# Kernel tuning notes

Measured on AMD Instinct MI355X. Metric: run time of the kernel, lower is better.

The kernel has to match this reference:

```python
import jax, jax.numpy as jnp
import numpy as np

B, L, N_PATCH, NUM_Q, C_IN, C_OUT = 32, 40, 2304, 100, 768, 256


def setup_inputs() -> dict:
    key = jax.random.key(0)
    ks = jax.random.split(key, 7)
    text_feat = jax.random.normal(ks[0], (B, L, C_IN), jnp.float32)
    img_feat = jax.random.normal(ks[1], (B, N_PATCH, C_IN), jnp.float32)
    # text_scores in (0,1): scale fns use log(1.22 - x), valid for x < 1.22
    text_scores = jax.random.uniform(ks[2], (B, 1), jnp.float32, 0.01, 0.99)
    text_mask = jax.random.randint(ks[3], (B, L), 0, 2).astype(jnp.int32)
    # guarantee at least a few unmasked text tokens per row (avoid all -inf)
    text_mask = text_mask.at[:, :4].set(0)
    dummy_token = jax.random.normal(ks[4], (1, NUM_Q, C_IN), jnp.float32)
    Wq = jax.random.normal(ks[5], (C_OUT, C_IN), jnp.float32) / np.sqrt(C_IN).astype(np.float32)
    bq = jnp.zeros((C_OUT,), jnp.float32)
    return dict(text_feat=text_feat, img_feat=img_feat, text_scores=text_scores,
                text_mask=text_mask, dummy_token=dummy_token, Wq=Wq, bq=bq)


def _l2norm(x, eps=1e-8):
    n = jnp.linalg.norm(x, axis=-1, keepdims=True)
    return x / jnp.maximum(n, eps)


def reference(text_feat, img_feat, text_scores, text_mask, dummy_token, Wq, bq):
    b, n_patch, c = img_feat.shape
    num_q = dummy_token.shape[1]
    l = text_feat.shape[1]

    # img features with learned dummy tokens appended: [B, N+Q, C]
    img_all = jnp.concatenate(
        [img_feat, jnp.broadcast_to(dummy_token, (b, num_q, c))], axis=1)

    # cosine similarity between every (patch|dummy) and every text token: [B, N+Q, L]
    cos = jnp.einsum('bpc,blc->bpl', _l2norm(img_all), _l2norm(text_feat))
    sim_norm = (cos + 1.0) * 0.5

    # custom log-based scale factors from text confidence score ([B,1])
    log_term = jnp.log(1.22 - text_scores)            # [B, 1]
    not_dummy = -0.59 * log_term + 0.12               # applied to real patches
    dummy = 0.59 * log_term + 0.88                    # applied to dummy tokens
    scale_factor = jnp.concatenate(
        [jnp.broadcast_to(not_dummy[:, :, None], (b, n_patch, l)),
         jnp.broadcast_to(dummy[:, :, None], (b, num_q, l))], axis=1)

    scaled = scale_factor * sim_norm                  # [B, N+Q, L]
    scaled = jnp.where(text_mask[:, None, :].astype(bool), -jnp.inf, scaled)

    # masked max over text tokens, then topk over patches (+dummies)
    max_per_patch = jnp.max(scaled, axis=-1)          # [B, N+Q]
    _, topk_idx = jax.lax.top_k(max_per_patch, num_q)  # [B, Q]

    # gather selected features (equivalent to one-hot scatter + bmm in torch)
    selected = jnp.take_along_axis(img_all, topk_idx[:, :, None], axis=1)  # [B,Q,C]
    query = selected @ Wq.T + bq                      # [B, Q, C_OUT]
    return query, topk_idx, sim_norm, scaled
```

## Files before the change

### kernel.cpp

```cpp
#include <hip/hip_runtime.h>
#include <math.h>

#define B_    32
#define L_    40
#define PIMG  2304
#define NQ    100
#define PALL  2404
#define C_    768
#define COUT  256
#define NT    24
#define TP    64

#define NEG_INF (-__builtin_huge_valf())
#define MASK_SENTINEL (-3.0e38f)

typedef short s16x8 __attribute__((ext_vector_type(8)));
typedef float f32x4 __attribute__((ext_vector_type(4)));

#define BSTR 40

__device__ __forceinline__ unsigned cvtpk(float a, float b) {
    unsigned r;
    asm("v_cvt_pk_bf16_f32 %0, %1, %2" : "=v"(r) : "v"(a), "v"(b));
    return r;
}
__device__ __forceinline__ void cvt44u(float4 v, uint2* h, uint2* l) {
    unsigned h01 = cvtpk(v.x, v.y);
    unsigned h23 = cvtpk(v.z, v.w);
    *h = make_uint2(h01, h23);
    *l = make_uint2(
        cvtpk(v.x - __uint_as_float(h01 << 16), v.y - __uint_as_float(h01 & 0xFFFF0000u)),
        cvtpk(v.z - __uint_as_float(h23 << 16), v.w - __uint_as_float(h23 & 0xFFFF0000u)));
}
union U4S8 { uint4 u; s16x8 s; };
__device__ __forceinline__ void split8(float4 v0, float4 v1, s16x8& h, s16x8& l) {
    unsigned h0 = cvtpk(v0.x, v0.y);
    unsigned h1 = cvtpk(v0.z, v0.w);
    unsigned h2 = cvtpk(v1.x, v1.y);
    unsigned h3 = cvtpk(v1.z, v1.w);
    unsigned l0 = cvtpk(v0.x - __uint_as_float(h0 << 16), v0.y - __uint_as_float(h0 & 0xFFFF0000u));
    unsigned l1 = cvtpk(v0.z - __uint_as_float(h1 << 16), v0.w - __uint_as_float(h1 & 0xFFFF0000u));
    unsigned l2 = cvtpk(v1.x - __uint_as_float(h2 << 16), v1.y - __uint_as_float(h2 & 0xFFFF0000u));
    unsigned l3 = cvtpk(v1.z - __uint_as_float(h3 << 16), v1.w - __uint_as_float(h3 & 0xFFFF0000u));
    U4S8 uh; uh.u = make_uint4(h0, h1, h2, h3); h = uh.s;
    U4S8 ul; ul.u = make_uint4(l0, l1, l2, l3); l = ul.s;
}
__device__ __forceinline__ float dot4(float4 v) {
    return v.x * v.x + v.y * v.y + v.z * v.z + v.w * v.w;
}

__device__ __forceinline__ void gl16(const float* g, float* lds_base) {
#if __has_builtin(__builtin_amdgcn_global_load_lds)
    __builtin_amdgcn_global_load_lds(
        (const __attribute__((address_space(1))) void*)g,
        (__attribute__((address_space(3))) void*)lds_base, 16, 0, 0);
#else
    const int lane = threadIdx.x & 63;
    *(float4*)((char*)lds_base + lane * 16) = *(const float4*)g;
#endif
}

#define MFMA3(ACC, AH, AL, BH, BL) do { \
    ACC = __builtin_amdgcn_mfma_f32_16x16x32_bf16(AH, BH, ACC, 0, 0, 0); \
    ACC = __builtin_amdgcn_mfma_f32_16x16x32_bf16(AH, BL, ACC, 0, 0, 0); \
    ACC = __builtin_amdgcn_mfma_f32_16x16x32_bf16(AL, BH, ACC, 0, 0, 0); \
} while (0)

__global__ void k_textnorm(const float* __restrict__ text, float* __restrict__ invT,
                           const float* __restrict__ scores,
                           float* __restrict__ sA, float* __restrict__ sB) {
    int t    = threadIdx.x;
    if (blockIdx.x == 0 && t < B_) {
        float s  = scores[t];
        float lt = logf(1.22f - s);
        sA[t] = -0.59f * lt + 0.12f;
        sB[t] =  0.59f * lt + 0.88f;
    }
    int row  = blockIdx.x * 4 + (t >> 6);
    int lane = t & 63;
    const float* src = text + (size_t)row * C_;
    float ss = 0.f;
#pragma unroll
    for (int j = 0; j < 12; ++j) {
        float x = src[lane + 64 * j];
        ss += x * x;
    }
#pragma unroll
    for (int m = 1; m < 64; m <<= 1) ss += __shfl_xor(ss, m);
    if (lane == 0) invT[row] = 1.0f / fmaxf(sqrtf(ss), 1e-8f);
}

__global__ __launch_bounds__(256) void k_main(
    const float* __restrict__ img,  const float* __restrict__ dummy,
    const float* __restrict__ text, const float* __restrict__ invT,
    const int*  __restrict__ mask,  const float* __restrict__ scaleA,
    const float* __restrict__ scaleB, float* __restrict__ simn,
    float* __restrict__ scld, float* __restrict__ maxpp)
{
    __shared__ float  Af[2][TP * 32];
    __shared__ ushort Bh[2][L_][BSTR], Bl[2][L_][BSTR];
    __shared__ float  invT_s[48];
    __shared__ int    mask_s[48];

    const int t    = threadIdx.x;
    const int b    = blockIdx.y;
    const int p0   = blockIdx.x * TP;
    const int lane = t & 63, w = t >> 6;
    const int lr   = lane & 15, kg = lane >> 4;

    if (t < 48) {
        invT_s[t] = (t < L_) ? invT[b * L_ + t] : 0.f;
        mask_s[t] = (t < L_) ? mask[b * L_ + t] : 1;
    }

    const float sA = scaleA[b], sB = scaleB[b];

    const int drow = lane >> 3, dchk = lane & 7;
    const int r0 = w * 16 + drow, r1 = r0 + 8;
    const int g0 = dchk ^ (r0 & 7), g1 = dchk ^ (r1 & 7);
    const int pA0 = min(p0 + r0, PALL - 1), pA1 = min(p0 + r1, PALL - 1);
    const float* gp0 = ((pA0 < PIMG) ? img + ((size_t)b * PIMG + pA0) * C_
                                     : dummy + (size_t)(pA0 - PIMG) * C_) + g0 * 4;
    const float* gp1 = ((pA1 < PIMG) ? img + ((size_t)b * PIMG + pA1) * C_
                                     : dummy + (size_t)(pA1 - PIMG) * C_) + g1 * 4;

    const int bl = t >> 2, bq = t & 3;
    const float* bbase = (t < 160) ? text + ((size_t)b * L_ + bl) * C_ + bq * 8 : nullptr;

    f32x4 acc[3];
#pragma unroll
    for (int ct = 0; ct < 3; ++ct) acc[ct] = (f32x4){0.f, 0.f, 0.f, 0.f};
    float nrm = 0.f;

    auto STAGE_A = [&](int it, int buf) {
        gl16(gp0 + it * 32, &Af[buf][(w * 16) * 32]);
        gl16(gp1 + it * 32, &Af[buf][(w * 16 + 8) * 32]);
    };
    auto LOADB = [&](int it, float4& v0, float4& v1) {
        if (bbase) {
            v0 = *(const float4*)(bbase + it * 32);
            v1 = *(const float4*)(bbase + it * 32 + 4);
        }
    };
    auto STOREB = [&](int buf, float4 v0, float4 v1) {
        if (bbase) {
            uint2 h, l;
            cvt44u(v0, &h, &l);
            { int q = bq * 2,     c = (q & 3) * 8 + (q >> 2) * 4;
              *(uint2*)&Bh[buf][bl][c] = h; *(uint2*)&Bl[buf][bl][c] = l; }
            cvt44u(v1, &h, &l);
            { int q = bq * 2 + 1, c = (q & 3) * 8 + (q >> 2) * 4;
              *(uint2*)&Bh[buf][bl][c] = h; *(uint2*)&Bl[buf][bl][c] = l; }
        }
    };
    auto COMPUTE = [&](int buf) {
        const int row = w * 16 + lr;
        const char* arow = (const char*)&Af[buf][row * 32];
        const int sw8 = row & 7;
        float4 va0 = *(const float4*)(arow + ((kg ^ sw8) << 4));
        float4 va1 = *(const float4*)(arow + (((4 + kg) ^ sw8) << 4));
        nrm += dot4(va0) + dot4(va1);
        s16x8 ah, al;
        split8(va0, va1, ah, al);
#pragma unroll
        for (int ct = 0; ct < 3; ++ct) {
            const int brow = min(ct * 16 + lr, L_ - 1);
            s16x8 bh  = *(const s16x8*)&Bh[buf][brow][kg * 8];
            s16x8 blo = *(const s16x8*)&Bl[buf][brow][kg * 8];
            MFMA3(acc[ct], ah, al, bh, blo);
        }
    };

    float4 xb0, xb1, yb0, yb1;
    STAGE_A(0, 0);
    LOADB(0, xb0, xb1);
    STOREB(0, xb0, xb1);
    LOADB(1, yb0, yb1);
    __syncthreads();

    for (int it = 0; it < NT; it += 2) {
        if (it + 1 < NT) { STAGE_A(it + 1, 1); STOREB(1, yb0, yb1); }
        if (it + 2 < NT) LOADB(it + 2, xb0, xb1);
        COMPUTE(0);
        __syncthreads();

        if (it + 2 < NT) { STAGE_A(it + 2, 0); STOREB(0, xb0, xb1); }
        if (it + 3 < NT) LOADB(it + 3, yb0, yb1);
        if (it + 1 < NT) COMPUTE(1);
        __syncthreads();
    }

    nrm += __shfl_xor(nrm, 16);
    nrm += __shfl_xor(nrm, 32);

#pragma unroll
    for (int reg = 0; reg < 4; ++reg) {
        const float ss   = __shfl(nrm, kg * 4 + reg);
        const float invn = 1.f / fmaxf(sqrtf(ss), 1e-8f);
        const int rloc = w * 16 + kg * 4 + reg;
        const int pp   = p0 + rloc;
        float mrow = NEG_INF;
        if (pp < PALL) {
            const float scl = (pp < PIMG) ? sA : sB;
            const size_t obase = ((size_t)b * PALL + pp) * L_;
#pragma unroll
            for (int ct = 0; ct < 3; ++ct) {
                const int col = ct * 16 + lr;
                float cosv = acc[ct][reg] * invn * invT_s[col];
                float sim  = (cosv + 1.f) * 0.5f;
                float sc   = mask_s[col] ? MASK_SENTINEL : scl * sim;
                if (col < L_) {
                    simn[obase + col] = sim;
                    scld[obase + col] = sc;
                    mrow = fmaxf(mrow, sc);
                }
            }
        }
        mrow = fmaxf(mrow, __shfl_xor(mrow, 1));
        mrow = fmaxf(mrow, __shfl_xor(mrow, 2));
        mrow = fmaxf(mrow, __shfl_xor(mrow, 4));
        mrow = fmaxf(mrow, __shfl_xor(mrow, 8));
        if (lr == 0 && pp < PALL) maxpp[b * PALL + pp] = mrow;
    }
}

__global__ __launch_bounds__(256) void k_rank(const float* __restrict__ maxpp,
                                              int* __restrict__ tki,
                                              float* __restrict__ topkf)
{
    __shared__ unsigned long long keys[PALL] __attribute__((aligned(16)));
    const int t = threadIdx.x;
    const int b = blockIdx.y;
    const int base = blockIdx.x * 512;
    const float* src = maxpp + (size_t)b * PALL;

    for (int i = t; i < PALL; i += 256) {
        unsigned u = __float_as_uint(src[i]);
        u = (u & 0x80000000u) ? ~u : (u | 0x80000000u);
        keys[i] = ((unsigned long long)u << 32) | (unsigned)(~i);
    }
    __syncthreads();

    const int i0 = base + t, i1 = base + t + 256;
    const unsigned long long k0 = (i0 < PALL) ? keys[i0] : ~0ull;
    const unsigned long long k1 = (i1 < PALL) ? keys[i1] : ~0ull;
    int c0 = 0, c1 = 0;
#pragma unroll 8
    for (int j = 0; j < PALL; j += 2) {
        ulonglong2 kk = *(const ulonglong2*)&keys[j];
        c0 += (kk.x > k0); c0 += (kk.y > k0);
        c1 += (kk.x > k1); c1 += (kk.y > k1);
    }
    if (i0 < PALL && c0 < NQ) { tki[b * NQ + c0] = i0; topkf[b * NQ + c0] = (float)i0; }
    if (i1 < PALL && c1 < NQ) { tki[b * NQ + c1] = i1; topkf[b * NQ + c1] = (float)i1; }
}

__global__ __launch_bounds__(256) void k_query(
    const float* __restrict__ img, const float* __restrict__ dummy,
    const float* __restrict__ Wq,  const float* __restrict__ bqv,
    const int*  __restrict__ tki,  float* __restrict__ query)
{
    __shared__ ushort Ah[2][64][BSTR], Al[2][64][BSTR];
    __shared__ ushort Bh[2][32][BSTR], Bl[2][32][BSTR];
    __shared__ const float* rowp[64];

    const int t    = threadIdx.x, lane = t & 63, w = t >> 6;
    const int lr   = lane & 15, kg = lane >> 4;
    const int rb   = blockIdx.x * 64, cb = blockIdx.y * 32;

    if (t < 64) {
        int R = rb + t; int sel = tki[R]; int bb = R / NQ;
        rowp[t] = (sel < PIMG) ? img + ((size_t)bb * PIMG + sel) * C_
                               : dummy + (size_t)(sel - PIMG) * C_;
    }
    __syncthreads();

    const int sr = t >> 2, sh = t & 3;
    const float* abase = rowp[sr] + sh * 8;
    const float* bbase = (t < 128) ? Wq + (size_t)(cb + (t >> 2)) * C_ + (t & 3) * 8 : nullptr;
    const int bl = t >> 2, bq = t & 3;

    f32x4 acc[2];
#pragma unroll
    for (int ct = 0; ct < 2; ++ct) acc[ct] = (f32x4){0.f, 0.f, 0.f, 0.f};

#define LOADQ(IT, A0, A1, Bv0, Bv1) do { \
        const int k0_ = (IT) * 32; \
        A0 = *(const float4*)(abase + k0_); \
        A1 = *(const float4*)(abase + k0_ + 4); \
        if (bbase) { \
            Bv0 = *(const float4*)(bbase + k0_); \
            Bv1 = *(const float4*)(bbase + k0_ + 4); \
        } \
    } while (0)

    auto STORE = [&](ushort (*AhD)[BSTR], ushort (*AlD)[BSTR],
                     ushort (*BhD)[BSTR], ushort (*BlD)[BSTR],
                     float4 A0, float4 A1, float4 Bv0, float4 Bv1) {
        uint2 h, l;
        cvt44u(A0, &h, &l);
        {
            const int q = sh * 2, col = (q & 3) * 8 + (q >> 2) * 4;
            *(uint2*)&AhD[sr][col] = h; *(uint2*)&AlD[sr][col] = l;
        }
        cvt44u(A1, &h, &l);
        {
            const int q = sh * 2 + 1, col = (q & 3) * 8 + (q >> 2) * 4;
            *(uint2*)&AhD[sr][col] = h; *(uint2*)&AlD[sr][col] = l;
        }
        if (bbase) {
            cvt44u(Bv0, &h, &l);
            {
                const int q = bq * 2, col = (q & 3) * 8 + (q >> 2) * 4;
                *(uint2*)&BhD[bl][col] = h; *(uint2*)&BlD[bl][col] = l;
            }
            cvt44u(Bv1, &h, &l);
            {
                const int q = bq * 2 + 1, col = (q & 3) * 8 + (q >> 2) * 4;
                *(uint2*)&BhD[bl][col] = h; *(uint2*)&BlD[bl][col] = l;
            }
        }
    };
    auto COMPUTE = [&](ushort (*AhS)[BSTR], ushort (*AlS)[BSTR],
                       ushort (*BhS)[BSTR], ushort (*BlS)[BSTR]) {
        const int row = w * 16 + lr;
        s16x8 ah = *(const s16x8*)&AhS[row][kg * 8];
        s16x8 al = *(const s16x8*)&AlS[row][kg * 8];
#pragma unroll
        for (int ct = 0; ct < 2; ++ct) {
            s16x8 bh  = *(const s16x8*)&BhS[ct * 16 + lr][kg * 8];
            s16x8 blo = *(const s16x8*)&BlS[ct * 16 + lr][kg * 8];
            MFMA3(acc[ct], ah, al, bh, blo);
        }
    };

    float4 xa0, xa1, xb0, xb1, ya0, ya1, yb0, yb1;
    LOADQ(0, xa0, xa1, xb0, xb1);
    STORE(Ah[0], Al[0], Bh[0], Bl[0], xa0, xa1, xb0, xb1);
    __syncthreads();

    for (int it = 0; it < NT; it += 2) {
        LOADQ(it + 1, ya0, ya1, yb0, yb1);
        COMPUTE(Ah[0], Al[0], Bh[0], Bl[0]);
        STORE(Ah[1], Al[1], Bh[1], Bl[1], ya0, ya1, yb0, yb1);
        __syncthreads();

        if (it + 2 < NT) LOADQ(it + 2, xa0, xa1, xb0, xb1);
        COMPUTE(Ah[1], Al[1], Bh[1], Bl[1]);
        if (it + 2 < NT) STORE(Ah[0], Al[0], Bh[0], Bl[0], xa0, xa1, xb0, xb1);
        __syncthreads();
    }
#undef LOADQ

#pragma unroll
    for (int reg = 0; reg < 4; ++reg) {
        const int R = rb + w * 16 + kg * 4 + reg;
#pragma unroll
        for (int ct = 0; ct < 2; ++ct) {
            const int col = cb + ct * 16 + lr;
            query[(size_t)R * COUT + col] = acc[ct][reg] + bqv[col];
        }
    }
}

extern "C" void kernel_launch(void* const* d_in, const int* in_sizes, int n_in,
                              void* d_out, int out_size, void* d_ws, size_t ws_size,
                              hipStream_t stream) {
    const float* text   = (const float*)d_in[0];
    const float* img    = (const float*)d_in[1];
    const float* scores = (const float*)d_in[2];
    const int*   mask   = (const int*)  d_in[3];
    const float* dummy  = (const float*)d_in[4];
    const float* Wq     = (const float*)d_in[5];
    const float* bq     = (const float*)d_in[6];

    float* out   = (float*)d_out;
    float* query = out;
    float* topkf = out + 819200;
    float* simn  = out + 822400;
    float* scld  = out + 3899520;

    float* wsf   = (float*)d_ws;
    float* invT  = wsf;
    float* sA    = wsf + 1280;
    float* sB    = wsf + 1312;
    float* maxpp = wsf + 1344;
    int*   tki   = (int*)(wsf + 78272);

    hipLaunchKernelGGL(k_textnorm, dim3(320),    dim3(256), 0, stream,
                       text, invT, scores, sA, sB);
    hipLaunchKernelGGL(k_main,     dim3(38, 32), dim3(256), 0, stream,
                       img, dummy, text, invT, mask, sA, sB, simn, scld, maxpp);
    hipLaunchKernelGGL(k_rank,     dim3(5, 32),  dim3(256), 0, stream, maxpp, tki, topkf);
    hipLaunchKernelGGL(k_query,    dim3(50, 8),  dim3(256), 0, stream,
                       img, dummy, Wq, bq, tki, query);
}
```

Baseline: 130.8 us.

## Stage query GEMM tiles as fp32 via direct global-to-LDS loads with XOR swizzle

The gathered-row query GEMM now copies raw fp32 tiles straight into shared memory with global-to-LDS loads (gl16) and an XOR-swizzled layout. Previously data passed through registers and was split into bf16 hi/lo halves before storing. The hi/lo split now happens after reading from shared memory, just before the MFMA. This is meant to cut register staging and conversion work on the load path and to avoid bank conflicts, at the cost of more shared-memory bytes per tile and split work repeated on every compute step.

```diff
diff --git a/kernel.cpp b/kernel.cpp
--- a/kernel.cpp
+++ b/kernel.cpp
@@ -260,8 +260,8 @@
     const float* __restrict__ Wq,  const float* __restrict__ bqv,
     const int*  __restrict__ tki,  float* __restrict__ query)
 {
-    __shared__ ushort Ah[2][64][BSTR], Al[2][64][BSTR];
-    __shared__ ushort Bh[2][32][BSTR], Bl[2][32][BSTR];
+    __shared__ float Af[2][64 * 32];
+    __shared__ float Bf[2][32 * 32];
     __shared__ const float* rowp[64];
 
     const int t    = threadIdx.x, lane = t & 63, w = t >> 6;
@@ -275,82 +275,53 @@
     }
     __syncthreads();
 
-    const int sr = t >> 2, sh = t & 3;
-    const float* abase = rowp[sr] + sh * 8;
-    const float* bbase = (t < 128) ? Wq + (size_t)(cb + (t >> 2)) * C_ + (t & 3) * 8 : nullptr;
-    const int bl = t >> 2, bq = t & 3;
+    const int drow = lane >> 3, dchk = lane & 7;
+    const float* gpA0 = rowp[w * 16 + drow]     + (dchk ^ drow) * 4;
+    const float* gpA1 = rowp[w * 16 + 8 + drow] + (dchk ^ drow) * 4;
+    const float* gpB  = Wq + (size_t)(cb + w * 8 + drow) * C_ + (dchk ^ drow) * 4;
 
     f32x4 acc[2];
 #pragma unroll
     for (int ct = 0; ct < 2; ++ct) acc[ct] = (f32x4){0.f, 0.f, 0.f, 0.f};
 
-#define LOADQ(IT, A0, A1, Bv0, Bv1) do { \
-        const int k0_ = (IT) * 32; \
-        A0 = *(const float4*)(abase + k0_); \
-        A1 = *(const float4*)(abase + k0_ + 4); \
-        if (bbase) { \
-            Bv0 = *(const float4*)(bbase + k0_); \
-            Bv1 = *(const float4*)(bbase + k0_ + 4); \
-        } \
-    } while (0)
-
-    auto STORE = [&](ushort (*AhD)[BSTR], ushort (*AlD)[BSTR],
-                     ushort (*BhD)[BSTR], ushort (*BlD)[BSTR],
-                     float4 A0, float4 A1, float4 Bv0, float4 Bv1) {
-        uint2 h, l;
-        cvt44u(A0, &h, &l);
-        {
-            const int q = sh * 2, col = (q & 3) * 8 + (q >> 2) * 4;
-            *(uint2*)&AhD[sr][col] = h; *(uint2*)&AlD[sr][col] = l;
-        }
-        cvt44u(A1, &h, &l);
-        {
-            const int q = sh * 2 + 1, col = (q & 3) * 8 + (q >> 2) * 4;
-            *(uint2*)&AhD[sr][col] = h; *(uint2*)&AlD[sr][col] = l;
-        }
-        if (bbase) {
-            cvt44u(Bv0, &h, &l);
-            {
-                const int q = bq * 2, col = (q & 3) * 8 + (q >> 2) * 4;
-                *(uint2*)&BhD[bl][col] = h; *(uint2*)&BlD[bl][col] = l;
-            }
-            cvt44u(Bv1, &h, &l);
-            {
-                const int q = bq * 2 + 1, col = (q & 3) * 8 + (q >> 2) * 4;
-                *(uint2*)&BhD[bl][col] = h; *(uint2*)&BlD[bl][col] = l;
-            }
-        }
-    };
-    auto COMPUTE = [&](ushort (*AhS)[BSTR], ushort (*AlS)[BSTR],
-                       ushort (*BhS)[BSTR], ushort (*BlS)[BSTR]) {
+    auto STAGE = [&](int it, int buf) {
+        gl16(gpA0 + it * 32, &Af[buf][(w * 16) * 32]);
+        gl16(gpA1 + it * 32, &Af[buf][(w * 16 + 8) * 32]);
+        gl16(gpB  + it * 32, &Bf[buf][(w * 8) * 32]);
+    };
+    auto COMPUTE = [&](int buf) {
         const int row = w * 16 + lr;
-        s16x8 ah = *(const s16x8*)&AhS[row][kg * 8];
-        s16x8 al = *(const s16x8*)&AlS[row][kg * 8];
+        const int sw8 = row & 7;
+        const float* arow = &Af[buf][row * 32];
+        float4 va0 = *(const float4*)(arow + (kg ^ sw8) * 4);
+        float4 va1 = *(const float4*)(arow + ((4 + kg) ^ sw8) * 4);
+        s16x8 ah, al;
+        split8(va0, va1, ah, al);
 #pragma unroll
         for (int ct = 0; ct < 2; ++ct) {
-            s16x8 bh  = *(const s16x8*)&BhS[ct * 16 + lr][kg * 8];
-            s16x8 blo = *(const s16x8*)&BlS[ct * 16 + lr][kg * 8];
-            MFMA3(acc[ct], ah, al, bh, blo);
-        }
-    };
-
-    float4 xa0, xa1, xb0, xb1, ya0, ya1, yb0, yb1;
-    LOADQ(0, xa0, xa1, xb0, xb1);
-    STORE(Ah[0], Al[0], Bh[0], Bl[0], xa0, xa1, xb0, xb1);
+            const int br  = ct * 16 + lr;
+            const int bs8 = br & 7;
+            const float* brow = &Bf[buf][br * 32];
+            float4 vb0 = *(const float4*)(brow + (kg ^ bs8) * 4);
+            float4 vb1 = *(const float4*)(brow + ((4 + kg) ^ bs8) * 4);
+            s16x8 bh, bl;
+            split8(vb0, vb1, bh, bl);
+            MFMA3(acc[ct], ah, al, bh, bl);
+        }
+    };
+
+    STAGE(0, 0);
     __syncthreads();
 
     for (int it = 0; it < NT; it += 2) {
-        LOADQ(it + 1, ya0, ya1, yb0, yb1);
-        COMPUTE(Ah[0], Al[0], Bh[0], Bl[0]);
-        STORE(Ah[1], Al[1], Bh[1], Bl[1], ya0, ya1, yb0, yb1);
+        if (it + 1 < NT) STAGE(it + 1, 1);
+        COMPUTE(0);
         __syncthreads();
 
-        if (it + 2 < NT) LOADQ(it + 2, xa0, xa1, xb0, xb1);
-        COMPUTE(Ah[1], Al[1], Bh[1], Bl[1]);
-        if (it + 2 < NT) STORE(Ah[0], Al[0], Bh[0], Bl[0], xa0, xa1, xb0, xb1);
+        if (it + 2 < NT) STAGE(it + 2, 0);
+        if (it + 1 < NT) COMPUTE(1);
         __syncthreads();
     }
-#undef LOADQ
 
 #pragma unroll
     for (int reg = 0; reg < 4; ++reg) {
```

After: 127.2 us. -2.7%, faster.
